# Optimization experiments

Hardware: AMD Instinct MI355X
Metric: run time of the kernel (lower is better)

The kernel has to match this reference:

```python
import jax, jax.numpy as jnp
import numpy as np

B, L, S, D, H = 2, 2048, 2048, 256, 8
HD = D // H  # per-head dim = 32
EPS = 1e-5


def _layernorm(x, g, b):
    m = jnp.mean(x, axis=-1, keepdims=True)
    v = jnp.mean(jnp.square(x - m), axis=-1, keepdims=True)
    return (x - m) * jax.lax.rsqrt(v + EPS) * g + b


def setup_inputs() -> dict:
    key = jax.random.key(0)
    ks = jax.random.split(key, 12)
    w = lambda k, o, i: jax.random.normal(k, (o, i), dtype=jnp.float32) * (1.0 / np.sqrt(i))
    return {
        "x": jax.random.normal(ks[0], (B, L, D), dtype=jnp.float32),
        "source": jax.random.normal(ks[1], (B, S, D), dtype=jnp.float32),
        "attn_factor": jax.random.uniform(ks[2], (B, L, S), dtype=jnp.float32),
        "Wq": w(ks[3], D, D),
        "Wk": w(ks[4], D, D),
        "Wv": w(ks[5], D, D),
        "Wm": w(ks[6], D, D),
        "W1": w(ks[7], 2 * D, 2 * D),
        "W2": w(ks[8], D, 2 * D),
        "g1": jnp.ones((D,), jnp.float32),
        "b1": jnp.zeros((D,), jnp.float32),
        "g2": jnp.ones((D,), jnp.float32),
        "b2": jnp.zeros((D,), jnp.float32),
    }


def reference(x, source, attn_factor, Wq, Wk, Wv, Wm, W1, W2, g1, b1, g2, b2):
    bs, l, d = x.shape
    s = source.shape[1]
    # projections (torch Linear: y = x @ W^T), split heads
    qw = (x @ Wq.T).reshape(bs, l, H, HD)       # [B,L,H,hd]
    kw = (source @ Wk.T).reshape(bs, s, H, HD)  # [B,S,H,hd]
    vw = (source @ Wv.T).reshape(bs, s, H, HD)  # [B,S,H,hd]
    # QK^T -> [B,L,S,H], scale, elementwise attn_factor, softmax over S
    a = jnp.einsum("nlhd,nshd->nlsh", qw, kw)
    a = a / np.sqrt(HD)
    a = a * attn_factor[:, :, :, None]
    a = jax.nn.softmax(a, axis=2)
    # AV -> [B,L,H,hd] -> merge heads
    o = jnp.einsum("nlsh,nshd->nlhd", a, vw).reshape(bs, l, d)
    message = o @ Wm.T
    message = _layernorm(message, g1, b1)
    h = jnp.concatenate([x, message], axis=2)       # [B,L,2D]
    h = jnp.maximum(h @ W1.T, 0.0)                  # ReLU MLP
    message = h @ W2.T                              # [B,L,D]
    message = _layernorm(message, g2, b2)
    return x + message
```

## Files before the change

### kernel.cpp

```cpp
#include <hip/hip_runtime.h>
#include <hip/hip_bf16.h>
#include <math.h>

#define B_  2
#define L_  2048
#define S_  2048
#define D_  256
#define H_  8
#define HD_ 32
#define ML_ (B_ * L_)
#define MS_ (B_ * S_)
#define NSPLIT 4
#define SCHUNK (S_ / NSPLIT)

typedef __attribute__((ext_vector_type(8))) short short8;
typedef __attribute__((ext_vector_type(4))) float f32x4;

__global__ __launch_bounds__(256) void convert_all(
    const float* __restrict__ x,  const float* __restrict__ src,
    const float* __restrict__ Wq, const float* __restrict__ Wk,
    const float* __restrict__ Wv, const float* __restrict__ Wm,
    const float* __restrict__ W1, const float* __restrict__ W2,
    __hip_bfloat16* xb,  __hip_bfloat16* srcb,
    __hip_bfloat16* Wqb, __hip_bfloat16* Wkb,
    __hip_bfloat16* Wvb, __hip_bfloat16* Wmb,
    __hip_bfloat16* W1b, __hip_bfloat16* W2b) {
    const size_t i4 = ((size_t)blockIdx.x * 256 + threadIdx.x) * 4;
    const float* sp; __hip_bfloat16* dp; size_t off;
    if      (i4 < 1048576) { sp = x;   dp = xb;   off = i4; }
    else if (i4 < 2097152) { sp = src; dp = srcb; off = i4 - 1048576; }
    else if (i4 < 2162688) { sp = Wq;  dp = Wqb;  off = i4 - 2097152; }
    else if (i4 < 2228224) { sp = Wk;  dp = Wkb;  off = i4 - 2162688; }
    else if (i4 < 2293760) { sp = Wv;  dp = Wvb;  off = i4 - 2228224; }
    else if (i4 < 2359296) { sp = Wm;  dp = Wmb;  off = i4 - 2293760; }
    else if (i4 < 2621440) { sp = W1;  dp = W1b;  off = i4 - 2359296; }
    else                   { sp = W2;  dp = W2b;  off = i4 - 2621440; }
    float4 v = *(const float4*)(sp + off);
    __hip_bfloat16 o0 = __float2bfloat16(v.x), o1 = __float2bfloat16(v.y);
    __hip_bfloat16 o2 = __float2bfloat16(v.z), o3 = __float2bfloat16(v.w);
    __hip_bfloat16* d = dp + off;
    d[0] = o0; d[1] = o1; d[2] = o2; d[3] = o3;
}

template <bool RELU, typename OutT>
__device__ __forceinline__ void gemm_body(const __hip_bfloat16* __restrict__ A,
                                          const __hip_bfloat16* __restrict__ A2,
                                          const __hip_bfloat16* __restrict__ Bm,
                                          OutT* __restrict__ C,
                                          int N, int K, int lda, int m0, int n0,
                                          float cscale,
                                          __hip_bfloat16 (&As)[64][72],
                                          __hip_bfloat16 (&Bs)[64][72]) {
    const int tid  = threadIdx.x;
    const int w    = tid >> 6;
    const int lane = tid & 63;
    const int colL = lane & 15;
    const int quad = lane >> 4;
    const int mh = (w & 1) * 32, nh = (w >> 1) * 32;
    const int srow = tid >> 3;
    const int scg  = (tid & 7) * 8;

    f32x4 acc[2][2] = {};

    auto loadA = [&](int p, int k0) -> short8 {
        const __hip_bfloat16* Asrc = A; int kk = k0;
        if (A2 && k0 >= 256) { Asrc = A2; kk = k0 - 256; }
        return *(const short8*)(Asrc + (size_t)(m0 + srow + p * 32) * lda + kk + scg);
    };
    auto loadB = [&](int p, int k0) -> short8 {
        return *(const short8*)(Bm + (size_t)(n0 + srow + p * 32) * K + k0 + scg);
    };

    short8 ra[2], rb[2];
#pragma unroll
    for (int p = 0; p < 2; ++p) { ra[p] = loadA(p, 0); rb[p] = loadB(p, 0); }

    for (int k0 = 0; k0 < K; k0 += 64) {
        __syncthreads();
#pragma unroll
        for (int p = 0; p < 2; ++p) {
            *(short8*)&As[srow + p * 32][scg] = ra[p];
            *(short8*)&Bs[srow + p * 32][scg] = rb[p];
        }
        __syncthreads();
        if (k0 + 64 < K) {
#pragma unroll
            for (int p = 0; p < 2; ++p) { ra[p] = loadA(p, k0 + 64); rb[p] = loadB(p, k0 + 64); }
        }
#pragma unroll
        for (int ks = 0; ks < 2; ++ks) {
            short8 af[2], bf[2];
#pragma unroll
            for (int i = 0; i < 2; ++i)
                af[i] = *(const short8*)&As[mh + i * 16 + colL][ks * 32 + quad * 8];
#pragma unroll
            for (int j = 0; j < 2; ++j)
                bf[j] = *(const short8*)&Bs[nh + j * 16 + colL][ks * 32 + quad * 8];
#pragma unroll
            for (int i = 0; i < 2; ++i)
#pragma unroll
                for (int j = 0; j < 2; ++j)
                    acc[i][j] = __builtin_amdgcn_mfma_f32_16x16x32_bf16(af[i], bf[j], acc[i][j], 0, 0, 0);
        }
    }
#pragma unroll
    for (int i = 0; i < 2; ++i)
#pragma unroll
        for (int r = 0; r < 4; ++r) {
            const size_t row = m0 + mh + i * 16 + quad * 4 + r;
#pragma unroll
            for (int j = 0; j < 2; ++j) {
                float v = acc[i][j][r] * cscale;
                if (RELU) v = fmaxf(v, 0.f);
                C[row * N + n0 + nh + j * 16 + colL] = (OutT)v;
            }
        }
}

template <bool RELU, typename OutT>
__global__ __launch_bounds__(256) void gemm_bf16(const __hip_bfloat16* __restrict__ A,
                                                 const __hip_bfloat16* __restrict__ A2,
                                                 const __hip_bfloat16* __restrict__ Bm,
                                                 OutT* __restrict__ C,
                                                 int N, int K, int lda) {
    __shared__ __hip_bfloat16 As[64][72];
    __shared__ __hip_bfloat16 Bs[64][72];
    gemm_body<RELU, OutT>(A, A2, Bm, C, N, K, lda,
                          blockIdx.x * 64, blockIdx.y * 64, 1.f, As, Bs);
}

__global__ __launch_bounds__(256) void proj_fused(const __hip_bfloat16* __restrict__ x_b,
                                                  const __hip_bfloat16* __restrict__ src_b,
                                                  const __hip_bfloat16* __restrict__ Wq_b,
                                                  const __hip_bfloat16* __restrict__ Wk_b,
                                                  const __hip_bfloat16* __restrict__ Wv_b,
                                                  __hip_bfloat16* __restrict__ Qb,
                                                  __hip_bfloat16* __restrict__ Kb,
                                                  __hip_bfloat16* __restrict__ Vtb) {
    __shared__ __hip_bfloat16 As[64][72];
    __shared__ __hip_bfloat16 Bs[64][72];
    const int id = blockIdx.x;
    if (id < 256) {
        gemm_body<false, __hip_bfloat16>(x_b, nullptr, Wq_b, Qb, 256, 256, 256,
                                         (id >> 2) * 64, (id & 3) * 64,
                                         0.17677669529663687f, As, Bs);
    } else if (id < 512) {
        const int t = id - 256;
        gemm_body<false, __hip_bfloat16>(src_b, nullptr, Wk_b, Kb, 256, 256, 256,
                                         (t >> 2) * 64, (t & 3) * 64, 1.f, As, Bs);
    } else {
        const int t = id - 512;
        const int b = t >> 7, u = t & 127;
        gemm_body<false, __hip_bfloat16>(Wv_b, nullptr, src_b + (size_t)b * S_ * D_,
                                         Vtb + (size_t)b * D_ * S_, S_, 256, 256,
                                         (u & 3) * 64, (u >> 2) * 64, 1.f, As, Bs);
    }
}

__global__ __launch_bounds__(256, 4) void attn_mfma(const __hip_bfloat16* __restrict__ Qb,
                                                    const __hip_bfloat16* __restrict__ Kb,
                                                    const __hip_bfloat16* __restrict__ Vtb,
                                                    const float* __restrict__ F,
                                                    __hip_bfloat16* __restrict__ Op,
                                                    float* __restrict__ Ll) {
    const int tid  = threadIdx.x;
    const int w    = tid >> 6;
    const int lane = tid & 63;
    const int colL = lane & 15;
    const int quad = lane >> 4;

    const int b     = blockIdx.z >> 2;
    const int split = blockIdx.z & 3;
    const int h     = blockIdx.y;
    const int qw    = blockIdx.x * 64 + w * 16;

    __shared__ __hip_bfloat16 Ks[128][40];
    __shared__ __hip_bfloat16 Vs[32][136];
    __shared__ __hip_bfloat16 Pw[4][16][72];

    const short8 aq = *(const short8*)(Qb + ((size_t)(b * L_ + qw + colL)) * D_ + h * HD_ + quad * 8);

    float lsum[4] = {0.f, 0.f, 0.f, 0.f};
    f32x4 o0 = {0.f, 0.f, 0.f, 0.f}, o1 = {0.f, 0.f, 0.f, 0.f};

    const int kr = tid >> 2, kc = (tid & 3) * 8;
    const int vr = tid >> 3, vc = (tid & 7) * 8;
    const __hip_bfloat16* kst = Kb + ((size_t)(b * S_ + kr)) * D_ + h * HD_ + kc;
    const __hip_bfloat16* vst = Vtb + (size_t)b * D_ * S_ + ((size_t)(h * HD_ + vr)) * S_ + vc;
    const float* fbase = F + ((size_t)(b * L_ + qw + quad * 4)) * S_ + colL;

    const int sbeg = split * SCHUNK, send = sbeg + SCHUNK;
    short8 rk[2], rv[2];
#pragma unroll
    for (int p = 0; p < 2; ++p) {
        rk[p] = *(const short8*)(kst + (size_t)(sbeg + p * 64) * D_);
        rv[p] = *(const short8*)(vst + sbeg + p * 64);
    }

    for (int s0 = sbeg; s0 < send; s0 += 128) {
        __syncthreads();
        *(short8*)&Ks[kr][kc]        = rk[0];
        *(short8*)&Ks[kr + 64][kc]   = rk[1];
        *(short8*)&Vs[vr][vc]        = rv[0];
        *(short8*)&Vs[vr][vc + 64]   = rv[1];
        __syncthreads();
        if (s0 + 128 < send) {
#pragma unroll
            for (int p = 0; p < 2; ++p) {
                rk[p] = *(const short8*)(kst + (size_t)(s0 + 128 + p * 64) * D_);
                rv[p] = *(const short8*)(vst + s0 + 128 + p * 64);
            }
        }
#pragma unroll
        for (int hs = 0; hs < 2; ++hs) {
            const int sh = s0 + hs * 64;
            f32x4 cc[4];
#pragma unroll
            for (int n = 0; n < 4; ++n) {
                short8 kf = *(const short8*)&Ks[hs * 64 + n * 16 + colL][quad * 8];
                f32x4 z = {0.f, 0.f, 0.f, 0.f};
                cc[n] = __builtin_amdgcn_mfma_f32_16x16x32_bf16(aq, kf, z, 0, 0, 0);
            }
#pragma unroll
            for (int n = 0; n < 4; ++n)
#pragma unroll
                for (int r = 0; r < 4; ++r) {
                    float fv = fbase[(size_t)r * S_ + sh + n * 16];
                    float p = __expf(cc[n][r] * fv);
                    lsum[r] += p;
                    Pw[w][quad * 4 + r][n * 16 + colL] = __float2bfloat16(p);
                }
            short8 a0 = *(const short8*)(&Pw[w][colL][quad * 8]);
            short8 a1 = *(const short8*)(&Pw[w][colL][32 + quad * 8]);
#pragma unroll
            for (int ks = 0; ks < 2; ++ks) {
                short8 ap = ks ? a1 : a0;
#pragma unroll
                for (int nt = 0; nt < 2; ++nt) {
                    short8 vf = *(const short8*)&Vs[nt * 16 + colL][hs * 64 + ks * 32 + quad * 8];
                    if (nt == 0) o0 = __builtin_amdgcn_mfma_f32_16x16x32_bf16(ap, vf, o0, 0, 0, 0);
                    else         o1 = __builtin_amdgcn_mfma_f32_16x16x32_bf16(ap, vf, o1, 0, 0, 0);
                }
            }
        }
    }

#pragma unroll
    for (int r = 0; r < 4; ++r) {
        float t = lsum[r];
        t += __shfl_xor(t, 1);
        t += __shfl_xor(t, 2);
        t += __shfl_xor(t, 4);
        t += __shfl_xor(t, 8);
        lsum[r] = t;
    }

#pragma unroll
    for (int r = 0; r < 4; ++r) {
        const size_t row = (size_t)(b * L_ + qw + quad * 4 + r);
        const size_t po = ((size_t)split * ML_ + row) * D_ + h * HD_;
        Op[po + colL]      = __float2bfloat16(o0[r]);
        Op[po + 16 + colL] = __float2bfloat16(o1[r]);
        if (colL == 0)
            Ll[((size_t)split * H_ + h) * ML_ + row] = lsum[r];
    }
}

__global__ __launch_bounds__(256) void gemm_ln_att(const __hip_bfloat16* __restrict__ Opart,
                                                   const float* __restrict__ Ll,
                                                   const __hip_bfloat16* __restrict__ Bm,
                                                   const float* __restrict__ g,
                                                   const float* __restrict__ bb,
                                                   __hip_bfloat16* __restrict__ Y) {
    __shared__ __hip_bfloat16 As[16][72];
    __shared__ __hip_bfloat16 Bs[256][72];
    __shared__ float gs[256], bs_[256];
    __shared__ float stats[4][16][2];
    __shared__ float Linv[16][8];
    const int tid  = threadIdx.x;
    const int w    = tid >> 6;
    const int lane = tid & 63;
    const int colL = lane & 15;
    const int quad = lane >> 4;
    const int nh = w * 64;
    const int m0 = blockIdx.x * 16;
    const int srow = tid >> 3;
    const int scg  = (tid & 7) * 8;
    const int K = 256;

    gs[tid] = g[tid]; bs_[tid] = bb[tid];
    if (tid < 128) {
        const int row = tid >> 3, hh = tid & 7;
        float t = 0.f;
#pragma unroll
        for (int s = 0; s < NSPLIT; ++s)
            t += Ll[((size_t)s * H_ + hh) * ML_ + m0 + row];
        Linv[row][hh] = 1.f / t;
    }
    __syncthreads();

    f32x4 acc[4] = {};

    auto loadA = [&](int k0) -> short8 {
        const float inv = Linv[srow][(k0 + scg) >> 5];
        float a[8] = {};
#pragma unroll
        for (int s = 0; s < NSPLIT; ++s) {
            short8 v = *(const short8*)(Opart + ((size_t)s * ML_ + m0 + srow) * 256 + k0 + scg);
#pragma unroll
            for (int e = 0; e < 8; ++e) {
                union { short s16; __hip_bfloat16 h; } c; c.s16 = v[e];
                a[e] += __bfloat162float(c.h);
            }
        }
        short8 outv;
#pragma unroll
        for (int e = 0; e < 8; ++e) {
            union { __hip_bfloat16 h; short s16; } c;
            c.h = __float2bfloat16(a[e] * inv);
            outv[e] = c.s16;
        }
        return outv;
    };
    auto loadB = [&](int p, int k0) -> short8 {
        return *(const short8*)(Bm + (size_t)(srow + p * 32) * K + k0 + scg);
    };

    short8 ra = {};
    if (srow < 16) ra = loadA(0);
    short8 rb[8];
#pragma unroll
    for (int p = 0; p < 8; ++p) rb[p] = loadB(p, 0);

    for (int k0 = 0; k0 < K; k0 += 64) {
        __syncthreads();
        if (srow < 16) *(short8*)&As[srow][scg] = ra;
#pragma unroll
        for (int p = 0; p < 8; ++p)
            *(short8*)&Bs[srow + p * 32][scg] = rb[p];
        __syncthreads();
        if (k0 + 64 < K) {
            if (srow < 16) ra = loadA(k0 + 64);
#pragma unroll
            for (int p = 0; p < 8; ++p) rb[p] = loadB(p, k0 + 64);
        }
#pragma unroll
        for (int ks = 0; ks < 2; ++ks) {
            short8 af = *(const short8*)&As[colL][ks * 32 + quad * 8];
#pragma unroll
            for (int j = 0; j < 4; ++j) {
                short8 bf = *(const short8*)&Bs[nh + j * 16 + colL][ks * 32 + quad * 8];
                acc[j] = __builtin_amdgcn_mfma_f32_16x16x32_bf16(af, bf, acc[j], 0, 0, 0);
            }
        }
    }

#pragma unroll
    for (int r = 0; r < 4; ++r) {
        float s = 0.f, q = 0.f;
#pragma unroll
        for (int j = 0; j < 4; ++j) {
            float v = acc[j][r];
            s += v; q += v * v;
        }
        s += __shfl_xor(s, 1); q += __shfl_xor(q, 1);
        s += __shfl_xor(s, 2); q += __shfl_xor(q, 2);
        s += __shfl_xor(s, 4); q += __shfl_xor(q, 4);
        s += __shfl_xor(s, 8); q += __shfl_xor(q, 8);
        if (colL == 0) {
            stats[w][quad * 4 + r][0] = s;
            stats[w][quad * 4 + r][1] = q;
        }
    }
    __syncthreads();

#pragma unroll
    for (int r = 0; r < 4; ++r) {
        const int row = quad * 4 + r;
        const float S = stats[0][row][0] + stats[1][row][0] + stats[2][row][0] + stats[3][row][0];
        const float Q = stats[0][row][1] + stats[1][row][1] + stats[2][row][1] + stats[3][row][1];
        const float mean = S * (1.f / 256.f);
        const float var  = Q * (1.f / 256.f) - mean * mean;
        const float rstd = rsqrtf(var + 1e-5f);
        const size_t grow = (size_t)(m0 + row) * 256;
#pragma unroll
        for (int j = 0; j < 4; ++j) {
            const int col = nh + j * 16 + colL;
            Y[grow + col] = __float2bfloat16((acc[j][r] - mean) * rstd * gs[col] + bs_[col]);
        }
    }
}

template <typename OutT>
__global__ __launch_bounds__(256) void gemm_ln(const __hip_bfloat16* __restrict__ A,
                                               const __hip_bfloat16* __restrict__ Bm,
                                               const float* __restrict__ g,
                                               const float* __restrict__ bb,
                                               const float* __restrict__ resid,
                                               OutT* __restrict__ Y,
                                               int K) {
    __shared__ __hip_bfloat16 As[16][72];
    __shared__ __hip_bfloat16 Bs[256][72];
    __shared__ float gs[256], bs_[256];
    __shared__ float stats[4][16][2];
    const int tid  = threadIdx.x;
    const int w    = tid >> 6;
    const int lane = tid & 63;
    const int colL = lane & 15;
    const int quad = lane >> 4;
    const int nh = w * 64;
    const int m0 = blockIdx.x * 16;
    const int srow = tid >> 3;
    const int scg  = (tid & 7) * 8;

    gs[tid] = g[tid]; bs_[tid] = bb[tid];

    f32x4 acc[4] = {};

    auto loadA = [&](int k0) -> short8 {
        return *(const short8*)(A + (size_t)(m0 + srow) * K + k0 + scg);
    };
    auto loadB = [&](int p, int k0) -> short8 {
        return *(const short8*)(Bm + (size_t)(srow + p * 32) * K + k0 + scg);
    };

    short8 ra = {};
    if (srow < 16) ra = loadA(0);
    short8 rb[8];
#pragma unroll
    for (int p = 0; p < 8; ++p) rb[p] = loadB(p, 0);

    for (int k0 = 0; k0 < K; k0 += 64) {
        __syncthreads();
        if (srow < 16) *(short8*)&As[srow][scg] = ra;
#pragma unroll
        for (int p = 0; p < 8; ++p)
            *(short8*)&Bs[srow + p * 32][scg] = rb[p];
        __syncthreads();
        if (k0 + 64 < K) {
            if (srow < 16) ra = loadA(k0 + 64);
#pragma unroll
            for (int p = 0; p < 8; ++p) rb[p] = loadB(p, k0 + 64);
        }
#pragma unroll
        for (int ks = 0; ks < 2; ++ks) {
            short8 af = *(const short8*)&As[colL][ks * 32 + quad * 8];
#pragma unroll
            for (int j = 0; j < 4; ++j) {
                short8 bf = *(const short8*)&Bs[nh + j * 16 + colL][ks * 32 + quad * 8];
                acc[j] = __builtin_amdgcn_mfma_f32_16x16x32_bf16(af, bf, acc[j], 0, 0, 0);
            }
        }
    }

#pragma unroll
    for (int r = 0; r < 4; ++r) {
        float s = 0.f, q = 0.f;
#pragma unroll
        for (int j = 0; j < 4; ++j) {
            float v = acc[j][r];
            s += v; q += v * v;
        }
        s += __shfl_xor(s, 1); q += __shfl_xor(q, 1);
        s += __shfl_xor(s, 2); q += __shfl_xor(q, 2);
        s += __shfl_xor(s, 4); q += __shfl_xor(q, 4);
        s += __shfl_xor(s, 8); q += __shfl_xor(q, 8);
        if (colL == 0) {
            stats[w][quad * 4 + r][0] = s;
            stats[w][quad * 4 + r][1] = q;
        }
    }
    __syncthreads();

#pragma unroll
    for (int r = 0; r < 4; ++r) {
        const int row = quad * 4 + r;
        const float S = stats[0][row][0] + stats[1][row][0] + stats[2][row][0] + stats[3][row][0];
        const float Q = stats[0][row][1] + stats[1][row][1] + stats[2][row][1] + stats[3][row][1];
        const float mean = S * (1.f / 256.f);
        const float var  = Q * (1.f / 256.f) - mean * mean;
        const float rstd = rsqrtf(var + 1e-5f);
        const size_t grow = (size_t)(m0 + row) * 256;
#pragma unroll
        for (int j = 0; j < 4; ++j) {
            const int col = nh + j * 16 + colL;
            float y = (acc[j][r] - mean) * rstd * gs[col] + bs_[col];
            if (resid) y += resid[grow + col];
            Y[grow + col] = (OutT)y;
        }
    }
}

extern "C" void kernel_launch(void* const* d_in, const int* in_sizes, int n_in,
                              void* d_out, int out_size, void* d_ws, size_t ws_size,
                              hipStream_t stream) {
    (void)in_sizes; (void)n_in; (void)out_size; (void)ws_size;
    const float* x   = (const float*)d_in[0];
    const float* src = (const float*)d_in[1];
    const float* F   = (const float*)d_in[2];
    const float* Wq  = (const float*)d_in[3];
    const float* Wk  = (const float*)d_in[4];
    const float* Wv  = (const float*)d_in[5];
    const float* Wm  = (const float*)d_in[6];
    const float* W1  = (const float*)d_in[7];
    const float* W2  = (const float*)d_in[8];
    const float* g1  = (const float*)d_in[9];
    const float* b1  = (const float*)d_in[10];
    const float* g2  = (const float*)d_in[11];
    const float* b2  = (const float*)d_in[12];
    float* out = (float*)d_out;

    char* ws = (char*)d_ws;
    __hip_bfloat16* x_b   = (__hip_bfloat16*)(ws);
    __hip_bfloat16* src_b = (__hip_bfloat16*)(ws + (2u << 20));
    __hip_bfloat16* Wq_b  = (__hip_bfloat16*)(ws + (4u << 20));
    __hip_bfloat16* Wk_b  = (__hip_bfloat16*)(ws + (4u << 20) + 131072);
    __hip_bfloat16* Wv_b  = (__hip_bfloat16*)(ws + (4u << 20) + 2 * 131072);
    __hip_bfloat16* Wm_b  = (__hip_bfloat16*)(ws + (4u << 20) + 3 * 131072);
    __hip_bfloat16* W1_b  = (__hip_bfloat16*)(ws + (4u << 20) + 4 * 131072);
    __hip_bfloat16* W2_b  = (__hip_bfloat16*)(ws + (4u << 20) + 4 * 131072 + 524288);
    __hip_bfloat16* Qb   = (__hip_bfloat16*)(ws + (6u << 20));
    __hip_bfloat16* Kb   = (__hip_bfloat16*)(ws + (8u << 20));
    __hip_bfloat16* Vtb  = (__hip_bfloat16*)(ws + (10u << 20));
    __hip_bfloat16* m1_b = (__hip_bfloat16*)(ws + (12u << 20));
    __hip_bfloat16* Opart = (__hip_bfloat16*)(ws + (14u << 20));
    float* Ll  = (float*)(ws + (22u << 20));
    __hip_bfloat16* h_b  = (__hip_bfloat16*)(ws + (20u << 20));

    dim3 blk(256);
    convert_all<<<dim3(2688), blk, 0, stream>>>(x, src, Wq, Wk, Wv, Wm, W1, W2,
                                                x_b, src_b, Wq_b, Wk_b, Wv_b, Wm_b, W1_b, W2_b);
    proj_fused<<<dim3(1024), blk, 0, stream>>>(x_b, src_b, Wq_b, Wk_b, Wv_b, Qb, Kb, Vtb);
    attn_mfma<<<dim3(L_ / 64, H_, B_ * NSPLIT), blk, 0, stream>>>(Qb, Kb, Vtb, F, Opart, Ll);
    gemm_ln_att<<<dim3(ML_ / 16), blk, 0, stream>>>(Opart, Ll, Wm_b, g1, b1, m1_b);
    gemm_bf16<true, __hip_bfloat16><<<dim3(ML_ / 64, 512 / 64), blk, 0, stream>>>(x_b, m1_b, W1_b, h_b, 512, 512, 256);
    gemm_ln<float><<<dim3(ML_ / 16), blk, 0, stream>>>(h_b, W2_b, g2, b2, x, out, 512);
}
```

Measured before the change: 164.2 us.

## Fuse merge projection, LayerNorm, MLP, and final LayerNorm into one kernel

New measurement: 161.5 us. About the same (-1.6%).

```diff
diff --git a/kernel.cpp b/kernel.cpp
--- a/kernel.cpp
+++ b/kernel.cpp
@@ -117,18 +117,6 @@
         }
 }
 
-template <bool RELU, typename OutT>
-__global__ __launch_bounds__(256) void gemm_bf16(const __hip_bfloat16* __restrict__ A,
-                                                 const __hip_bfloat16* __restrict__ A2,
-                                                 const __hip_bfloat16* __restrict__ Bm,
-                                                 OutT* __restrict__ C,
-                                                 int N, int K, int lda) {
-    __shared__ __hip_bfloat16 As[64][72];
-    __shared__ __hip_bfloat16 Bs[64][72];
-    gemm_body<RELU, OutT>(A, A2, Bm, C, N, K, lda,
-                          blockIdx.x * 64, blockIdx.y * 64, 1.f, As, Bs);
-}
-
 __global__ __launch_bounds__(256) void proj_fused(const __hip_bfloat16* __restrict__ x_b,
                                                   const __hip_bfloat16* __restrict__ src_b,
                                                   const __hip_bfloat16* __restrict__ Wq_b,
@@ -266,29 +254,37 @@
     }
 }
 
-__global__ __launch_bounds__(256) void gemm_ln_att(const __hip_bfloat16* __restrict__ Opart,
-                                                   const float* __restrict__ Ll,
-                                                   const __hip_bfloat16* __restrict__ Bm,
-                                                   const float* __restrict__ g,
-                                                   const float* __restrict__ bb,
-                                                   __hip_bfloat16* __restrict__ Y) {
+__global__ __launch_bounds__(256) void mlp_fused(const __hip_bfloat16* __restrict__ Opart,
+                                                 const float* __restrict__ Ll,
+                                                 const __hip_bfloat16* __restrict__ x_b,
+                                                 const __hip_bfloat16* __restrict__ Wm_b,
+                                                 const __hip_bfloat16* __restrict__ W1_b,
+                                                 const __hip_bfloat16* __restrict__ W2_b,
+                                                 const float* __restrict__ g1,
+                                                 const float* __restrict__ b1,
+                                                 const float* __restrict__ g2,
+                                                 const float* __restrict__ b2,
+                                                 const float* __restrict__ x,
+                                                 float* __restrict__ out) {
+    __shared__ __hip_bfloat16 Bs[256][72];
     __shared__ __hip_bfloat16 As[16][72];
-    __shared__ __hip_bfloat16 Bs[256][72];
+    __shared__ __hip_bfloat16 Acat[16][520];
+    __shared__ __hip_bfloat16 Hs[16][520];
     __shared__ float gs[256], bs_[256];
     __shared__ float stats[4][16][2];
     __shared__ float Linv[16][8];
+
     const int tid  = threadIdx.x;
     const int w    = tid >> 6;
     const int lane = tid & 63;
     const int colL = lane & 15;
     const int quad = lane >> 4;
-    const int nh = w * 64;
-    const int m0 = blockIdx.x * 16;
+    const int nh   = w * 64;
+    const int m0   = blockIdx.x * 16;
     const int srow = tid >> 3;
     const int scg  = (tid & 7) * 8;
-    const int K = 256;
-
-    gs[tid] = g[tid]; bs_[tid] = bb[tid];
+
+    gs[tid] = g1[tid]; bs_[tid] = b1[tid];
     if (tid < 128) {
         const int row = tid >> 3, hh = tid & 7;
         float t = 0.f;
@@ -297,11 +293,15 @@
             t += Ll[((size_t)s * H_ + hh) * ML_ + m0 + row];
         Linv[row][hh] = 1.f / t;
     }
+    {
+        const int xr = tid >> 4, xc = (tid & 15) * 16;
+        *(short8*)&Acat[xr][xc]     = *(const short8*)(x_b + (size_t)(m0 + xr) * 256 + xc);
+        *(short8*)&Acat[xr][xc + 8] = *(const short8*)(x_b + (size_t)(m0 + xr) * 256 + xc + 8);
+    }
     __syncthreads();
 
     f32x4 acc[4] = {};
-
-    auto loadA = [&](int k0) -> short8 {
+    auto loadA1 = [&](int k0) -> short8 {
         const float inv = Linv[srow][(k0 + scg) >> 5];
         float a[8] = {};
 #pragma unroll
@@ -322,171 +322,160 @@
         }
         return outv;
     };
-    auto loadB = [&](int p, int k0) -> short8 {
-        return *(const short8*)(Bm + (size_t)(srow + p * 32) * K + k0 + scg);
-    };
-
-    short8 ra = {};
-    if (srow < 16) ra = loadA(0);
-    short8 rb[8];
-#pragma unroll
-    for (int p = 0; p < 8; ++p) rb[p] = loadB(p, 0);
-
-    for (int k0 = 0; k0 < K; k0 += 64) {
-        __syncthreads();
-        if (srow < 16) *(short8*)&As[srow][scg] = ra;
+
+    {
+        short8 ra = {};
+        if (srow < 16) ra = loadA1(0);
+        short8 rb[8];
 #pragma unroll
         for (int p = 0; p < 8; ++p)
-            *(short8*)&Bs[srow + p * 32][scg] = rb[p];
-        __syncthreads();
-        if (k0 + 64 < K) {
-            if (srow < 16) ra = loadA(k0 + 64);
-#pragma unroll
-            for (int p = 0; p < 8; ++p) rb[p] = loadB(p, k0 + 64);
-        }
-#pragma unroll
-        for (int ks = 0; ks < 2; ++ks) {
-            short8 af = *(const short8*)&As[colL][ks * 32 + quad * 8];
-#pragma unroll
-            for (int j = 0; j < 4; ++j) {
-                short8 bf = *(const short8*)&Bs[nh + j * 16 + colL][ks * 32 + quad * 8];
-                acc[j] = __builtin_amdgcn_mfma_f32_16x16x32_bf16(af, bf, acc[j], 0, 0, 0);
-            }
-        }
-    }
-
+            rb[p] = *(const short8*)(Wm_b + (size_t)(srow + p * 32) * 256 + scg);
+        for (int k0 = 0; k0 < 256; k0 += 64) {
+            __syncthreads();
+            if (srow < 16) *(short8*)&As[srow][scg] = ra;
+#pragma unroll
+            for (int p = 0; p < 8; ++p)
+                *(short8*)&Bs[srow + p * 32][scg] = rb[p];
+            __syncthreads();
+            if (k0 + 64 < 256) {
+                if (srow < 16) ra = loadA1(k0 + 64);
+#pragma unroll
+                for (int p = 0; p < 8; ++p)
+                    rb[p] = *(const short8*)(Wm_b + (size_t)(srow + p * 32) * 256 + k0 + 64 + scg);
+            }
+#pragma unroll
+            for (int ks = 0; ks < 2; ++ks) {
+                short8 af = *(const short8*)&As[colL][ks * 32 + quad * 8];
+#pragma unroll
+                for (int j = 0; j < 4; ++j) {
+                    short8 bf = *(const short8*)&Bs[nh + j * 16 + colL][ks * 32 + quad * 8];
+                    acc[j] = __builtin_amdgcn_mfma_f32_16x16x32_bf16(af, bf, acc[j], 0, 0, 0);
+                }
+            }
+        }
+    }
 #pragma unroll
     for (int r = 0; r < 4; ++r) {
         float s = 0.f, q = 0.f;
 #pragma unroll
-        for (int j = 0; j < 4; ++j) {
-            float v = acc[j][r];
-            s += v; q += v * v;
-        }
+        for (int j = 0; j < 4; ++j) { float v = acc[j][r]; s += v; q += v * v; }
         s += __shfl_xor(s, 1); q += __shfl_xor(q, 1);
         s += __shfl_xor(s, 2); q += __shfl_xor(q, 2);
         s += __shfl_xor(s, 4); q += __shfl_xor(q, 4);
         s += __shfl_xor(s, 8); q += __shfl_xor(q, 8);
-        if (colL == 0) {
-            stats[w][quad * 4 + r][0] = s;
-            stats[w][quad * 4 + r][1] = q;
-        }
+        if (colL == 0) { stats[w][quad * 4 + r][0] = s; stats[w][quad * 4 + r][1] = q; }
     }
     __syncthreads();
-
 #pragma unroll
     for (int r = 0; r < 4; ++r) {
         const int row = quad * 4 + r;
         const float S = stats[0][row][0] + stats[1][row][0] + stats[2][row][0] + stats[3][row][0];
         const float Q = stats[0][row][1] + stats[1][row][1] + stats[2][row][1] + stats[3][row][1];
         const float mean = S * (1.f / 256.f);
-        const float var  = Q * (1.f / 256.f) - mean * mean;
-        const float rstd = rsqrtf(var + 1e-5f);
-        const size_t grow = (size_t)(m0 + row) * 256;
+        const float rstd = rsqrtf(Q * (1.f / 256.f) - mean * mean + 1e-5f);
 #pragma unroll
         for (int j = 0; j < 4; ++j) {
             const int col = nh + j * 16 + colL;
-            Y[grow + col] = __float2bfloat16((acc[j][r] - mean) * rstd * gs[col] + bs_[col]);
-        }
-    }
-}
-
-template <typename OutT>
-__global__ __launch_bounds__(256) void gemm_ln(const __hip_bfloat16* __restrict__ A,
-                                               const __hip_bfloat16* __restrict__ Bm,
-                                               const float* __restrict__ g,
-                                               const float* __restrict__ bb,
-                                               const float* __restrict__ resid,
-                                               OutT* __restrict__ Y,
-                                               int K) {
-    __shared__ __hip_bfloat16 As[16][72];
-    __shared__ __hip_bfloat16 Bs[256][72];
-    __shared__ float gs[256], bs_[256];
-    __shared__ float stats[4][16][2];
-    const int tid  = threadIdx.x;
-    const int w    = tid >> 6;
-    const int lane = tid & 63;
-    const int colL = lane & 15;
-    const int quad = lane >> 4;
-    const int nh = w * 64;
-    const int m0 = blockIdx.x * 16;
-    const int srow = tid >> 3;
-    const int scg  = (tid & 7) * 8;
-
-    gs[tid] = g[tid]; bs_[tid] = bb[tid];
-
-    f32x4 acc[4] = {};
-
-    auto loadA = [&](int k0) -> short8 {
-        return *(const short8*)(A + (size_t)(m0 + srow) * K + k0 + scg);
-    };
-    auto loadB = [&](int p, int k0) -> short8 {
-        return *(const short8*)(Bm + (size_t)(srow + p * 32) * K + k0 + scg);
-    };
-
-    short8 ra = {};
-    if (srow < 16) ra = loadA(0);
-    short8 rb[8];
-#pragma unroll
-    for (int p = 0; p < 8; ++p) rb[p] = loadB(p, 0);
-
-    for (int k0 = 0; k0 < K; k0 += 64) {
-        __syncthreads();
-        if (srow < 16) *(short8*)&As[srow][scg] = ra;
+            Acat[row][256 + col] = __float2bfloat16((acc[j][r] - mean) * rstd * gs[col] + bs_[col]);
+        }
+    }
+    __syncthreads();
+
+#pragma unroll 1
+    for (int nc = 0; nc < 2; ++nc) {
+#pragma unroll
+        for (int j = 0; j < 4; ++j) acc[j] = (f32x4){0.f, 0.f, 0.f, 0.f};
+        short8 rb[8];
 #pragma unroll
         for (int p = 0; p < 8; ++p)
-            *(short8*)&Bs[srow + p * 32][scg] = rb[p];
-        __syncthreads();
-        if (k0 + 64 < K) {
-            if (srow < 16) ra = loadA(k0 + 64);
-#pragma unroll
-            for (int p = 0; p < 8; ++p) rb[p] = loadB(p, k0 + 64);
-        }
-#pragma unroll
-        for (int ks = 0; ks < 2; ++ks) {
-            short8 af = *(const short8*)&As[colL][ks * 32 + quad * 8];
+            rb[p] = *(const short8*)(W1_b + (size_t)(nc * 256 + srow + p * 32) * 512 + scg);
+        for (int k0 = 0; k0 < 512; k0 += 64) {
+            __syncthreads();
+#pragma unroll
+            for (int p = 0; p < 8; ++p)
+                *(short8*)&Bs[srow + p * 32][scg] = rb[p];
+            __syncthreads();
+            if (k0 + 64 < 512) {
+#pragma unroll
+                for (int p = 0; p < 8; ++p)
+                    rb[p] = *(const short8*)(W1_b + (size_t)(nc * 256 + srow + p * 32) * 512 + k0 + 64 + scg);
+            }
+#pragma unroll
+            for (int ks = 0; ks < 2; ++ks) {
+                short8 af = *(const short8*)&Acat[colL][k0 + ks * 32 + quad * 8];
+#pragma unroll
+                for (int j = 0; j < 4; ++j) {
+                    short8 bf = *(const short8*)&Bs[nh + j * 16 + colL][ks * 32 + quad * 8];
+                    acc[j] = __builtin_amdgcn_mfma_f32_16x16x32_bf16(af, bf, acc[j], 0, 0, 0);
+                }
+            }
+        }
+#pragma unroll
+        for (int r = 0; r < 4; ++r) {
+            const int row = quad * 4 + r;
 #pragma unroll
             for (int j = 0; j < 4; ++j) {
-                short8 bf = *(const short8*)&Bs[nh + j * 16 + colL][ks * 32 + quad * 8];
-                acc[j] = __builtin_amdgcn_mfma_f32_16x16x32_bf16(af, bf, acc[j], 0, 0, 0);
-            }
-        }
-    }
-
+                const int col = nc * 256 + nh + j * 16 + colL;
+                Hs[row][col] = __float2bfloat16(fmaxf(acc[j][r], 0.f));
+            }
+        }
+    }
+    gs[tid] = g2[tid]; bs_[tid] = b2[tid];
+    __syncthreads();
+
+#pragma unroll
+    for (int j = 0; j < 4; ++j) acc[j] = (f32x4){0.f, 0.f, 0.f, 0.f};
+    {
+        short8 rb[8];
+#pragma unroll
+        for (int p = 0; p < 8; ++p)
+            rb[p] = *(const short8*)(W2_b + (size_t)(srow + p * 32) * 512 + scg);
+        for (int k0 = 0; k0 < 512; k0 += 64) {
+            __syncthreads();
+#pragma unroll
+            for (int p = 0; p < 8; ++p)
+                *(short8*)&Bs[srow + p * 32][scg] = rb[p];
+            __syncthreads();
+            if (k0 + 64 < 512) {
+#pragma unroll
+                for (int p = 0; p < 8; ++p)
+                    rb[p] = *(const short8*)(W2_b + (size_t)(srow + p * 32) * 512 + k0 + 64 + scg);
+            }
+#pragma unroll
+            for (int ks = 0; ks < 2; ++ks) {
+                short8 af = *(const short8*)&Hs[colL][k0 + ks * 32 + quad * 8];
+#pragma unroll
+                for (int j = 0; j < 4; ++j) {
+                    short8 bf = *(const short8*)&Bs[nh + j * 16 + colL][ks * 32 + quad * 8];
+                    acc[j] = __builtin_amdgcn_mfma_f32_16x16x32_bf16(af, bf, acc[j], 0, 0, 0);
+                }
+            }
+        }
+    }
 #pragma unroll
     for (int r = 0; r < 4; ++r) {
         float s = 0.f, q = 0.f;
 #pragma unroll
-        for (int j = 0; j < 4; ++j) {
-            float v = acc[j][r];
-            s += v; q += v * v;
-        }
+        for (int j = 0; j < 4; ++j) { float v = acc[j][r]; s += v; q += v * v; }
         s += __shfl_xor(s, 1); q += __shfl_xor(q, 1);
         s += __shfl_xor(s, 2); q += __shfl_xor(q, 2);
         s += __shfl_xor(s, 4); q += __shfl_xor(q, 4);
         s += __shfl_xor(s, 8); q += __shfl_xor(q, 8);
-        if (colL == 0) {
-            stats[w][quad * 4 + r][0] = s;
-            stats[w][quad * 4 + r][1] = q;
-        }
+        if (colL == 0) { stats[w][quad * 4 + r][0] = s; stats[w][quad * 4 + r][1] = q; }
     }
     __syncthreads();
-
 #pragma unroll
     for (int r = 0; r < 4; ++r) {
         const int row = quad * 4 + r;
         const float S = stats[0][row][0] + stats[1][row][0] + stats[2][row][0] + stats[3][row][0];
         const float Q = stats[0][row][1] + stats[1][row][1] + stats[2][row][1] + stats[3][row][1];
         const float mean = S * (1.f / 256.f);
-        const float var  = Q * (1.f / 256.f) - mean * mean;
-        const float rstd = rsqrtf(var + 1e-5f);
+        const float rstd = rsqrtf(Q * (1.f / 256.f) - mean * mean + 1e-5f);
         const size_t grow = (size_t)(m0 + row) * 256;
 #pragma unroll
         for (int j = 0; j < 4; ++j) {
             const int col = nh + j * 16 + colL;
-            float y = (acc[j][r] - mean) * rstd * gs[col] + bs_[col];
-            if (resid) y += resid[grow + col];
-            Y[grow + col] = (OutT)y;
+            out[grow + col] = (acc[j][r] - mean) * rstd * gs[col] + bs_[col] + x[grow + col];
         }
     }
 }
@@ -522,17 +511,14 @@
     __hip_bfloat16* Qb   = (__hip_bfloat16*)(ws + (6u << 20));
     __hip_bfloat16* Kb   = (__hip_bfloat16*)(ws + (8u << 20));
     __hip_bfloat16* Vtb  = (__hip_bfloat16*)(ws + (10u << 20));
-    __hip_bfloat16* m1_b = (__hip_bfloat16*)(ws + (12u << 20));
     __hip_bfloat16* Opart = (__hip_bfloat16*)(ws + (14u << 20));
     float* Ll  = (float*)(ws + (22u << 20));
-    __hip_bfloat16* h_b  = (__hip_bfloat16*)(ws + (20u << 20));
 
     dim3 blk(256);
     convert_all<<<dim3(2688), blk, 0, stream>>>(x, src, Wq, Wk, Wv, Wm, W1, W2,
                                                 x_b, src_b, Wq_b, Wk_b, Wv_b, Wm_b, W1_b, W2_b);
     proj_fused<<<dim3(1024), blk, 0, stream>>>(x_b, src_b, Wq_b, Wk_b, Wv_b, Qb, Kb, Vtb);
     attn_mfma<<<dim3(L_ / 64, H_, B_ * NSPLIT), blk, 0, stream>>>(Qb, Kb, Vtb, F, Opart, Ll);
-    gemm_ln_att<<<dim3(ML_ / 16), blk, 0, stream>>>(Opart, Ll, Wm_b, g1, b1, m1_b);
-    gemm_bf16<true, __hip_bfloat16><<<dim3(ML_ / 64, 512 / 64), blk, 0, stream>>>(x_b, m1_b, W1_b, h_b, 512, 512, 256);
-    gemm_ln<float><<<dim3(ML_ / 16), blk, 0, stream>>>(h_b, W2_b, g2, b2, x, out, 512);
+    mlp_fused<<<dim3(ML_ / 16), blk, 0, stream>>>(Opart, Ll, x_b, Wm_b, W1_b, W2_b,
+                                                  g1, b1, g2, b2, x, out);
 }
```
